# Kernel optimization log

Measured on AMD Instinct MI355X. Metric: run time of the kernel, lower is better.

## Reference

```python
import jax, jax.numpy as jnp
import numpy as np

NL, NQ, FD, HD, NH = 6, 128, 256, 512, 8
NC, B, T, H, W = 6, 1, 1, 48, 120
PPF = 24 // 6  # points_per_face
P = PPF * PPF * 6  # code emits (num_points//6)^2 points per face = 96 total
NPARAM, NTYPE, NATTR = 11, 10, 3
PMIN = np.array([-50., -50., -5., -15., -15., -5., -5., -3.14, 0.5, 0.5, 0.5], np.float32)
PMAX = np.array([50., 50., 5., 15., 15., 5., 5., 3.14, 10., 5., 3.], np.float32)


def _box_template():
    off = np.linspace(-0.4, 0.4, PPF).astype(np.float32)
    pts = []
    for axis in range(3):  # -x,+x,-y,+y,-z,+z faces, same order as torch code
        for s in (-0.5, 0.5):
            rem = [a for a in range(3) if a != axis]
            for i in range(PPF):
                for j in range(PPF):
                    p = [0.0, 0.0, 0.0]
                    p[axis] = s
                    p[rem[0]] = off[i]
                    p[rem[1]] = off[j]
                    pts.append(p)
    return np.asarray(pts, np.float32)  # [P,3]

TPL = _box_template()


def _mlp2(x, w1, b1, w2, b2):
    return jax.nn.relu(x @ w1.T + b1) @ w2.T + b2


def _ln(x, g, b):
    m = x.mean(-1, keepdims=True)
    v = ((x - m) ** 2).mean(-1, keepdims=True)
    return (x - m) * jax.lax.rsqrt(v + 1e-5) * g + b


def _mha(q, k, v, in_w, in_b, out_w, out_b):
    hd = HD // NH
    wq, wk, wv = jnp.split(in_w, 3, axis=0)
    bq, bk, bv = jnp.split(in_b, 3)
    def heads(x, w, b):
        y = x @ w.T + b
        return y.reshape(x.shape[0], x.shape[1], NH, hd).transpose(0, 2, 1, 3)
    Q, K, V = heads(q, wq, bq), heads(k, wk, bk), heads(v, wv, bv)
    a = jax.nn.softmax(jnp.einsum('bhqd,bhkd->bhqk', Q, K) * (hd ** -0.5), axis=-1)
    o = jnp.einsum('bhqk,bhkd->bhqd', a, V)
    o = o.transpose(0, 2, 1, 3).reshape(q.shape[0], q.shape[1], HD)
    return o @ out_w.T + out_b


def _sample_box_points(motion):
    # motion [B,N,11] -> [B,N,P,3]; indices: X0 Y1 Z2 .. YAW7 L8 W9 H10
    c = motion[..., 0:3]
    dims = motion[..., 8:11]
    yaw = motion[..., 7]
    p = TPL * dims[:, :, None, :]  # [B,N,P,3]
    cy, sy = jnp.cos(yaw)[..., None], jnp.sin(yaw)[..., None]
    xr = p[..., 0] * cy - p[..., 1] * sy
    yr = p[..., 0] * sy + p[..., 1] * cy
    return jnp.stack([xr, yr, p[..., 2]], -1) + c[:, :, None, :]


def _gather_aggregate(pts, features, proj):
    # pts [B,N,P,3]; features [NC,B,T,C,H,W]; proj [NC,3,4]
    Bb, N, Pp, _ = pts.shape
    NP = N * Pp
    hom = jnp.concatenate([pts, jnp.ones_like(pts[..., :1])], -1)
    feat_flat = features.reshape(NC, Bb, T, FD, H * W)
    acc = jnp.zeros((Bb, FD, NP), features.dtype)
    for cidx in range(NC):
        cam = jnp.einsum('ij,bnpj->bnpi', proj[cidx], hom)  # [B,N,P,3]
        z = cam[..., 2]
        zs = jnp.where(jnp.abs(z) > 1e-6, z, 1e-6)
        u = (cam[..., 0] / zs).reshape(Bb, NP)
        v = (cam[..., 1] / zs).reshape(Bb, NP)
        front = (z > 0).reshape(Bb, NP)
        u0, v0 = jnp.floor(u), jnp.floor(v)
        du, dv = u - u0, v - v0
        cam_acc = jnp.zeros((Bb, T, FD, NP), features.dtype)
        for (ui, vi, wgt) in ((u0, v0, (1 - du) * (1 - dv)),
                              (u0 + 1, v0, du * (1 - dv)),
                              (u0, v0 + 1, (1 - du) * dv),
                              (u0 + 1, v0 + 1, du * dv)):
            ok = front & (ui >= 0) & (ui <= W - 1) & (vi >= 0) & (vi <= H - 1)
            idx = (jnp.clip(vi, 0, H - 1) * W + jnp.clip(ui, 0, W - 1)).astype(jnp.int32)
            bidx = jnp.broadcast_to(idx[:, None, None, :], (Bb, T, FD, NP))
            g = jnp.take_along_axis(feat_flat[cidx], bidx, axis=-1)
            cam_acc = cam_acc + g * (wgt * ok)[:, None, None, :]
        acc = acc + cam_acc.mean(axis=1)  # mean over time
    agg = (acc / NC).reshape(Bb, FD, N, Pp).mean(-1)  # mean over cams and points
    return agg.transpose(0, 2, 1)  # [B,N,C]

_ga = jax.checkpoint(_gather_aggregate)


def _forward(features, proj, ego_states, queries0, param_min, param_max, motion_w1, motion_b1, motion_w2, motion_b2, type_w1, type_b1, type_w2, type_b2, attr_w1, attr_b1, attr_w2, attr_b2, fmlp_w1, fmlp_b1, fmlp_w2, fmlp_b2, sa_in_w, sa_in_b, sa_out_w, sa_out_b, fa_in_w, fa_in_b, fa_out_w, fa_out_b, ffn_w1, ffn_b1, ffn_w2, ffn_b2, ln1_g, ln1_b, ln2_g, ln2_b, ln3_g, ln3_b):
    Bb = features.shape[1]
    q = jnp.broadcast_to(queries0, (Bb, NQ, HD))
    preds = []
    for i in range(NL):
        motion = jax.nn.sigmoid(_mlp2(q, motion_w1, motion_b1, motion_w2, motion_b2)) * (param_max - param_min) + param_min
        tlog = _mlp2(q, type_w1, type_b1, type_w2, type_b2)
        attr = jax.nn.sigmoid(_mlp2(q, attr_w1, attr_b1, attr_w2, attr_b2))
        preds.append(jnp.concatenate([motion, tlog, attr], -1))
        if i == NL - 1:
            break  # last layer only predicts (layers[-1] unused, as in torch code)
        pts = _sample_box_points(motion)
        agg = _ga(pts, features, proj)
        feat_h = _mlp2(agg, fmlp_w1, fmlp_b1, fmlp_w2, fmlp_b2)
        x = _ln(q, ln1_g[i], ln1_b[i])
        x = x + _mha(x, x, x, sa_in_w[i], sa_in_b[i], sa_out_w[i], sa_out_b[i])
        x = _ln(x, ln2_g[i], ln2_b[i])
        x = x + _mha(x, feat_h, feat_h, fa_in_w[i], fa_in_b[i], fa_out_w[i], fa_out_b[i])
        x = _ln(x, ln3_g[i], ln3_b[i])
        q = x + _mlp2(x, ffn_w1[i], ffn_b1[i], ffn_w2[i], ffn_b2[i])
    return jnp.stack(preds)  # [NL,B,NQ,24]


def setup_inputs() -> dict:
    key = jax.random.key(0)
    ks = iter(jax.random.split(key, 64))
    def g(shape, s=0.02):
        return jax.random.normal(next(ks), shape, jnp.float32) * s
    fx, cx, cy = 40.0, W / 2.0, H / 2.0
    Ps = []
    for c in range(NC):
        th = 2.0 * np.pi * c / NC
        Rm = np.stack([np.array([-np.sin(th), np.cos(th), 0.0]),
                       np.array([0.0, 0.0, -1.0]),
                       np.array([np.cos(th), np.sin(th), 0.0])])
        K = np.array([[fx, 0.0, cx], [0.0, fx, cy], [0.0, 0.0, 1.0]])
        Pm = np.zeros((3, 4))
        Pm[:, :3] = K @ Rm
        Ps.append(Pm)
    inp = dict(
        features=jax.random.normal(next(ks), (NC, B, T, FD, H, W), jnp.float32),
        proj=jnp.asarray(np.asarray(Ps, np.float32)),
        ego_states=jax.random.normal(next(ks), (B, T, 5), jnp.float32),
        queries0=g((1, NQ, HD), 1.0),
        param_min=jnp.asarray(PMIN), param_max=jnp.asarray(PMAX),
        motion_w1=g((HD, HD)), motion_b1=jnp.zeros((HD,)),
        motion_w2=g((NPARAM, HD)), motion_b2=jnp.zeros((NPARAM,)),
        type_w1=g((HD, HD)), type_b1=jnp.zeros((HD,)),
        type_w2=g((NTYPE, HD)), type_b2=jnp.zeros((NTYPE,)),
        attr_w1=g((HD, HD)), attr_b1=jnp.zeros((HD,)),
        attr_w2=g((NATTR, HD)), attr_b2=jnp.zeros((NATTR,)),
        fmlp_w1=g((HD, FD)), fmlp_b1=jnp.zeros((HD,)),
        fmlp_w2=g((HD, HD)), fmlp_b2=jnp.zeros((HD,)),
        sa_in_w=g((NL, 3 * HD, HD)), sa_in_b=jnp.zeros((NL, 3 * HD)),
        sa_out_w=g((NL, HD, HD)), sa_out_b=jnp.zeros((NL, HD)),
        fa_in_w=g((NL, 3 * HD, HD)), fa_in_b=jnp.zeros((NL, 3 * HD)),
        fa_out_w=g((NL, HD, HD)), fa_out_b=jnp.zeros((NL, HD)),
        ffn_w1=g((NL, 4 * HD, HD)), ffn_b1=jnp.zeros((NL, 4 * HD)),
        ffn_w2=g((NL, HD, 4 * HD)), ffn_b2=jnp.zeros((NL, HD)),
        ln1_g=jnp.ones((NL, HD)), ln1_b=jnp.zeros((NL, HD)),
        ln2_g=jnp.ones((NL, HD)), ln2_b=jnp.zeros((NL, HD)),
        ln3_g=jnp.ones((NL, HD)), ln3_b=jnp.zeros((NL, HD)),
    )
    return inp


def reference(features, proj, ego_states, queries0, param_min, param_max, motion_w1, motion_b1, motion_w2, motion_b2, type_w1, type_b1, type_w2, type_b2, attr_w1, attr_b1, attr_w2, attr_b2, fmlp_w1, fmlp_b1, fmlp_w2, fmlp_b2, sa_in_w, sa_in_b, sa_out_w, sa_out_b, fa_in_w, fa_in_b, fa_out_w, fa_out_b, ffn_w1, ffn_b1, ffn_w2, ffn_b2, ln1_g, ln1_b, ln2_g, ln2_b, ln3_g, ln3_b):
    return _forward(features, proj, ego_states, queries0, param_min, param_max, motion_w1, motion_b1, motion_w2, motion_b2, type_w1, type_b1, type_w2, type_b2, attr_w1, attr_b1, attr_w2, attr_b2, fmlp_w1, fmlp_b1, fmlp_w2, fmlp_b2, sa_in_w, sa_in_b, sa_out_w, sa_out_b, fa_in_w, fa_in_b, fa_out_w, fa_out_b, ffn_w1, ffn_b1, ffn_w2, ffn_b2, ln1_g, ln1_b, ln2_g, ln2_b, ln3_g, ln3_b)
```

## Files before the change

kernel.cpp:

```cpp
#include <hip/hip_runtime.h>
#include <hip/hip_bf16.h>

typedef __hip_bfloat16 bf16;
typedef _Float16 h16;
typedef __attribute__((ext_vector_type(8))) _Float16 half8;
typedef __attribute__((ext_vector_type(4))) _Float16 half4;
typedef __attribute__((ext_vector_type(4))) float f32x4;

#define NQ 128
#define HD 512
#define FD 256
#define NC 6
#define IMH 48
#define IMW 120
#define HW 5760

__device__ __forceinline__ half8 pack8(float4 x, float4 y) {
    half8 h;
    h[0] = (h16)x.x; h[1] = (h16)x.y; h[2] = (h16)x.z; h[3] = (h16)x.w;
    h[4] = (h16)y.x; h[5] = (h16)y.y; h[6] = (h16)y.z; h[7] = (h16)y.w;
    return h;
}


__device__ __forceinline__ void transpose_body(int bx, int by, int cam,
                                               int tx, int ty, float* tile,
                                               const float* __restrict__ f,
                                               bf16* __restrict__ ft)
{
    int hw0 = bx * 32, fd0 = by * 32;
    const float* fb = f + (size_t)cam * FD * HW;
    for (int r = ty; r < 32; r += 8)
        tile[r * 33 + tx] = fb[(size_t)(fd0 + r) * HW + hw0 + tx];
    __syncthreads();
    bf16* fo = ft + (size_t)cam * HW * FD;
    for (int r = ty; r < 32; r += 8)
        fo[(size_t)(hw0 + r) * FD + fd0 + tx] = __float2bfloat16(tile[tx * 33 + r]);
}

struct SwzDesc {
    const float* src[11];
    unsigned int chunkStart[12];
    unsigned int tileStart[11];
    int K[11];
};

__device__ __forceinline__ int lperm(int lane, int ksl) {
    return lane ^ ((lane >> 4) & 3) ^ (ksl << 2);
}

__device__ __forceinline__ void swizzle_body(int bid, int t, h16* fbuf,
                                             const SwzDesc& d, h16* __restrict__ dst)
{
    int w = 0;
    while (bid >= (int)d.chunkStart[w + 1]) w++;
    int local = bid - (int)d.chunkStart[w];
    int Kk = d.K[w];
    int kc = Kk >> 6;
    int n64 = local / kc, kchunk = local - n64 * kc;

    int rr  = t >> 4;
    int cb  = (t & 15) * 4;
    int ksl = (t >> 3) & 1;
    int kk  = cb & 31;
    int laneb = ((kk >> 3) << 4) + rr;
    int elemB = (kk & 7) * 2;
    const float* sbase = d.src[w] + (size_t)(n64 * 64 + rr) * Kk + kchunk * 64 + cb;
#pragma unroll
    for (int rp = 0; rp < 4; rp++) {
        float4 u = *(const float4*)(sbase + (size_t)rp * 16 * Kk);
        int tile8 = ksl * 4 + rp;
        int l2 = lperm(laneb, ksl);
        half4* fp = (half4*)((char*)fbuf + tile8 * 1024 + l2 * 16 + elemB);
        half4 hv; hv[0] = (h16)u.x; hv[1] = (h16)u.y; hv[2] = (h16)u.z; hv[3] = (h16)u.w;
        *fp = hv;
    }
    __syncthreads();

    int K32 = Kk >> 5;
#pragma unroll
    for (int i = 0; i < 2; i++) {
        int hidx = t + i * 256;
        int tl = hidx >> 6, within = hidx & 63;
        int ksl2 = tl >> 2, ctt = tl & 3;
        int l2 = lperm(within, ksl2);
        size_t tileg = (size_t)d.tileStart[w]
                     + ((size_t)n64 * K32 + (kchunk * 2 + ksl2)) * 4 + ctt;
        *(half8*)(dst + tileg * 512 + within * 8) =
            *(const half8*)((const char*)fbuf + tl * 1024 + l2 * 16);
    }
}

template<int CTN, int NSUM, bool A2SW, bool LNA>
__device__ __forceinline__ void gemm_body(int bx, int by, int tid,
    float* redu, float* sst, float* sst2,
    const h16* __restrict__ A16, int lda, int sumStride,
    const float* __restrict__ A32,
    const float* __restrict__ lng, const float* __restrict__ lnb,
    float* __restrict__ lnout,
    const h16* __restrict__ A2_16, int a2Start,
    const h16* __restrict__ Wswz,
    const float* __restrict__ B0, const float* __restrict__ B1, const float* __restrict__ B2s,
    const float* __restrict__ R, int ldr,
    float* __restrict__ C32, h16* __restrict__ C16, int ldc,
    int K, int act)
{
    int w = tid >> 6, l = tid & 63;
    int lr = l & 15, q4 = l >> 4;
    int m0 = by * 16;
    int n0 = bx * 16 * CTN;
    int row = m0 + lr;
    int K32 = K >> 5;
    int KQ = K32 >> 2;
    int ks0 = w * KQ;

    bool useA2 = A2SW && (bx >= a2Start);

    const float* arow32 = nullptr;
    float mean = 0.f, rstd = 1.f;
    if (LNA && !useA2) {
        arow32 = A32 + (size_t)row * K + q4 * 8;
        float s = 0.f, s2 = 0.f;
        for (int ks = ks0; ks < ks0 + KQ; ks++) {
            float4 u = *(const float4*)(arow32 + ks * 32);
            float4 v = *(const float4*)(arow32 + ks * 32 + 4);
            s  += u.x + u.y + u.z + u.w + v.x + v.y + v.z + v.w;
            s2 += u.x*u.x + u.y*u.y + u.z*u.z + u.w*u.w
                + v.x*v.x + v.y*v.y + v.z*v.z + v.w*v.w;
        }
        s  += __shfl_xor(s, 16);  s  += __shfl_xor(s, 32);
        s2 += __shfl_xor(s2, 16); s2 += __shfl_xor(s2, 32);
        if (q4 == 0) { sst[w * 16 + lr] = s; sst2[w * 16 + lr] = s2; }
        __syncthreads();
        float st = sst[lr] + sst[16 + lr] + sst[32 + lr] + sst[48 + lr];
        float st2 = sst2[lr] + sst2[16 + lr] + sst2[32 + lr] + sst2[48 + lr];
        mean = st * (1.0f / (float)K);
        float var = st2 * (1.0f / (float)K) - mean * mean;
        rstd = rsqrtf(var + 1e-5f);
    }

    const h16* arow16 = nullptr;
    if (useA2)       arow16 = A2_16 + (size_t)row * 512 + q4 * 8;
    else if (!LNA)   arow16 = A16 + (size_t)row * lda + q4 * 8;

    const h16* wbase[CTN];
#pragma unroll
    for (int ct = 0; ct < CTN; ct++) {
        int tct = (n0 >> 4) + ct;
        wbase[ct] = Wswz + (((size_t)(tct >> 2) * K32 * 4 + (tct & 3)) * 64 + l) * 8;
    }

    f32x4 acc[CTN];
#pragma unroll
    for (int ct = 0; ct < CTN; ct++) acc[ct] = (f32x4){0.f, 0.f, 0.f, 0.f};

    bool wrln = LNA && !useA2 && (bx == 0) && lnout;

#pragma unroll 4
    for (int ks = ks0; ks < ks0 + KQ; ks++) {
        half8 a;
        if (LNA && !useA2) {
            float4 u = *(const float4*)(arow32 + ks * 32);
            float4 v = *(const float4*)(arow32 + ks * 32 + 4);
            float4 g0 = *(const float4*)(lng + ks * 32 + q4 * 8);
            float4 g1 = *(const float4*)(lng + ks * 32 + q4 * 8 + 4);
            float4 b0 = *(const float4*)(lnb + ks * 32 + q4 * 8);
            float4 b1 = *(const float4*)(lnb + ks * 32 + q4 * 8 + 4);
            float4 o0, o1;
            o0.x = (u.x - mean) * rstd * g0.x + b0.x;
            o0.y = (u.y - mean) * rstd * g0.y + b0.y;
            o0.z = (u.z - mean) * rstd * g0.z + b0.z;
            o0.w = (u.w - mean) * rstd * g0.w + b0.w;
            o1.x = (v.x - mean) * rstd * g1.x + b1.x;
            o1.y = (v.y - mean) * rstd * g1.y + b1.y;
            o1.z = (v.z - mean) * rstd * g1.z + b1.z;
            o1.w = (v.w - mean) * rstd * g1.w + b1.w;
            if (wrln) {
                *(float4*)(lnout + (size_t)row * K + ks * 32 + q4 * 8)     = o0;
                *(float4*)(lnout + (size_t)row * K + ks * 32 + q4 * 8 + 4) = o1;
            }
            a = pack8(o0, o1);
        } else if (NSUM == 1) {
            a = *(const half8*)(arow16 + (size_t)ks * 32);
        } else {
            float s[8] = {0.f, 0.f, 0.f, 0.f, 0.f, 0.f, 0.f, 0.f};
#pragma unroll
            for (int j = 0; j < NSUM; j++) {
                half8 tt = *(const half8*)(arow16 + (size_t)j * sumStride + ks * 32);
#pragma unroll
                for (int e = 0; e < 8; e++) s[e] += (float)tt[e];
            }
#pragma unroll
            for (int e = 0; e < 8; e++) a[e] = (h16)s[e];
        }
#pragma unroll
        for (int ct = 0; ct < CTN; ct++) {
            half8 bfr = *(const half8*)(wbase[ct] + (size_t)ks * 2048);
            acc[ct] = __builtin_amdgcn_mfma_f32_16x16x32_f16(a, bfr, acc[ct], 0, 0, 0);
        }
    }

#pragma unroll
    for (int ct = 0; ct < CTN; ct++)
        *(f32x4*)&redu[(size_t)(w * CTN + ct) * 256 + l * 4] = acc[ct];
    __syncthreads();

    if (w < CTN) {
        int ct = w;
        f32x4 sum = *(const f32x4*)&redu[(size_t)ct * 256 + l * 4];
#pragma unroll
        for (int w2 = 1; w2 < 4; w2++) {
            f32x4 tt = *(const f32x4*)&redu[(size_t)(w2 * CTN + ct) * 256 + l * 4];
            sum[0] += tt[0]; sum[1] += tt[1]; sum[2] += tt[2]; sum[3] += tt[3];
        }
        int n = n0 + ct * 16 + lr;
        float bv;
        if (B1) { int sec = n >> 9, ni = n & 511;
                  bv = (sec == 0) ? B0[ni] : (sec == 1 ? B1[ni] : B2s[ni]); }
        else bv = B0[n];
#pragma unroll
        for (int r = 0; r < 4; r++) {
            int m = m0 + q4 * 4 + r;
            float v = sum[r] + bv;
            if (act) v = fmaxf(v, 0.f);
            if (R) v += R[(size_t)m * ldr + n];
            if (C32) C32[(size_t)m * ldc + n] = v;
            if (C16) C16[(size_t)m * ldc + n] = (h16)v;
        }
    }
}

__device__ __forceinline__ void heads2_body(int q, int n, int lane,
    const h16* __restrict__ hid16,
    const float* __restrict__ w2m, const float* __restrict__ b2m,
    const float* __restrict__ w2t, const float* __restrict__ b2t,
    const float* __restrict__ w2a, const float* __restrict__ b2a,
    const float* __restrict__ pmin, const float* __restrict__ pmax,
    float* __restrict__ out)
{
    const float* wr; float bv; int mode, sect;
    if (n < 11)      { sect = 0; wr = w2m + n * 512;        bv = b2m[n];      mode = 0; }
    else if (n < 21) { sect = 1; wr = w2t + (n - 11) * 512; bv = b2t[n - 11]; mode = 1; }
    else             { sect = 2; wr = w2a + (n - 21) * 512; bv = b2a[n - 21]; mode = 2; }
    half8 hv = *(const half8*)(hid16 + q * 1536 + sect * 512 + lane * 8);
    const float4* w4 = (const float4*)(wr + lane * 8);
    float4 c0 = w4[0], c1 = w4[1];
    float acc = (float)hv[0] * c0.x + (float)hv[1] * c0.y
              + (float)hv[2] * c0.z + (float)hv[3] * c0.w
              + (float)hv[4] * c1.x + (float)hv[5] * c1.y
              + (float)hv[6] * c1.z + (float)hv[7] * c1.w;
    for (int off = 32; off; off >>= 1) acc += __shfl_xor(acc, off);
    if (lane == 0) {
        float v = acc + bv;
        if (mode == 0)      v = (1.0f / (1.0f + __expf(-v))) * (pmax[n] - pmin[n]) + pmin[n];
        else if (mode == 2) v = 1.0f / (1.0f + __expf(-v));
        out[q * 24 + n] = v;
    }
}

__device__ __forceinline__ void attn_body(int bid, int tid,
                                          float* KVl, float* Ql, float* Pl,
                                          const float* __restrict__ qkv,
                                          h16* __restrict__ out16)
{
    int h = bid >> 2, chunk = bid & 3;

    for (int l = tid; l < 2048; l += 256) {
        int row = l >> 4, c4 = (l & 15) * 4;
        float4 v = *(const float4*)&qkv[row * 1536 + 512 + h * 64 + c4];
        *(float4*)&KVl[row * 68 + c4] = v;
    }
    for (int l = tid; l < 512; l += 256) {
        int row = l >> 4, c4 = (l & 15) * 4;
        float4 v = *(const float4*)&qkv[(chunk * 32 + row) * 1536 + h * 64 + c4];
        *(float4*)&Ql[row * 68 + c4] = v;
    }
    __syncthreads();

    int w = tid >> 6, j = tid & 63;
    for (int r8 = 0; r8 < 8; r8++) {
        int lr = w * 8 + r8;
        float s0 = 0.f, s1 = 0.f;
#pragma unroll
        for (int k4 = 0; k4 < 64; k4 += 4) {
            float4 qv  = *(const float4*)&Ql[lr * 68 + k4];
            float4 k0v = *(const float4*)&KVl[j * 68 + k4];
            float4 k1v = *(const float4*)&KVl[(j + 64) * 68 + k4];
            s0 += qv.x * k0v.x + qv.y * k0v.y + qv.z * k0v.z + qv.w * k0v.w;
            s1 += qv.x * k1v.x + qv.y * k1v.y + qv.z * k1v.z + qv.w * k1v.w;
        }
        s0 *= 0.125f; s1 *= 0.125f;
        float m = fmaxf(s0, s1);
        for (int off = 32; off; off >>= 1) m = fmaxf(m, __shfl_xor(m, off));
        float e0 = __expf(s0 - m), e1 = __expf(s1 - m);
        float sm = e0 + e1;
        for (int off = 32; off; off >>= 1) sm += __shfl_xor(sm, off);
        float inv = 1.0f / sm;
        Pl[lr * 128 + j]      = e0 * inv;
        Pl[lr * 128 + j + 64] = e1 * inv;
    }
    __syncthreads();

    for (int l = tid; l < 2048; l += 256) {
        int row = l >> 4, c4 = (l & 15) * 4;
        float4 v = *(const float4*)&qkv[row * 1536 + 1024 + h * 64 + c4];
        KVl[(c4 + 0) * 132 + row] = v.x;
        KVl[(c4 + 1) * 132 + row] = v.y;
        KVl[(c4 + 2) * 132 + row] = v.z;
        KVl[(c4 + 3) * 132 + row] = v.w;
    }
    __syncthreads();

    int d = tid & 63, w2 = tid >> 6;
    for (int r8 = 0; r8 < 8; r8++) {
        int lr = w2 * 8 + r8;
        float o = 0.f;
#pragma unroll
        for (int j4 = 0; j4 < 128; j4 += 4) {
            float4 pv = *(const float4*)&Pl[lr * 128 + j4];
            float4 vv = *(const float4*)&KVl[d * 132 + j4];
            o += pv.x * vv.x + pv.y * vv.y + pv.z * vv.z + pv.w * vv.w;
        }
        out16[(chunk * 32 + lr) * 512 + h * 64 + d] = (h16)o;
    }
}


__global__ __launch_bounds__(256) void prep_k(SwzDesc d, h16* __restrict__ swz,
                                              const float* __restrict__ feat,
                                              bf16* __restrict__ feat_t,
                                              const float* __restrict__ q0,
                                              h16* __restrict__ q016)
{
    __shared__ char shm[8448];
    int bid = blockIdx.x, t = threadIdx.x;
    if (bid < 6432) {
        swizzle_body(bid, t, (h16*)shm, d, swz);
    } else if (bid < 15072) {
        int tb = bid - 6432;
        transpose_body(tb % 180, (tb / 180) % 8, tb / 1440, t & 31, t >> 5,
                       (float*)shm, feat, feat_t);
    } else {
        int i = (bid - 15072) * 256 + t;
        q016[i] = (h16)q0[i];
    }
}

template<int CTN, int NSUM, bool A2SW, bool LNA>
__global__ __launch_bounds__(256) void gemm_sk4(
    const h16* __restrict__ A16, int lda, int sumStride,
    const float* __restrict__ A32,
    const float* __restrict__ lng, const float* __restrict__ lnb,
    float* __restrict__ lnout,
    const h16* __restrict__ A2_16, int a2Start,
    const h16* __restrict__ Wswz,
    const float* __restrict__ B0, const float* __restrict__ B1, const float* __restrict__ B2s,
    const float* __restrict__ R, int ldr,
    float* __restrict__ C32, h16* __restrict__ C16, int ldc,
    int K, int act)
{
    __shared__ float redu[CTN * 4 * 256];
    __shared__ float sst[64], sst2[64];
    gemm_body<CTN, NSUM, A2SW, LNA>(blockIdx.x, blockIdx.y, threadIdx.x,
        redu, sst, sst2, A16, lda, sumStride, A32, lng, lnb, lnout, A2_16, a2Start,
        Wswz, B0, B1, B2s, R, ldr, C32, C16, ldc, K, act);
}

__global__ __launch_bounds__(64) void heads2_k(const h16* __restrict__ hid16,
                                               const float* __restrict__ w2m, const float* __restrict__ b2m,
                                               const float* __restrict__ w2t, const float* __restrict__ b2t,
                                               const float* __restrict__ w2a, const float* __restrict__ b2a,
                                               const float* __restrict__ pmin, const float* __restrict__ pmax,
                                               float* __restrict__ out)
{
    heads2_body(blockIdx.x, blockIdx.y, threadIdx.x,
                hid16, w2m, b2m, w2t, b2t, w2a, b2a, pmin, pmax, out);
}

__global__ __launch_bounds__(256) void attn_k(const float* __restrict__ qkv,
                                              h16* __restrict__ out16)
{
    __shared__ float KVl[128 * 68];
    __shared__ float Ql[32 * 68];
    __shared__ float Pl[32 * 128];
    attn_body(blockIdx.x, threadIdx.x, KVl, Ql, Pl, qkv, out16);
}

__global__ __launch_bounds__(256) void d2_k(
    const float* __restrict__ q32, const float* __restrict__ lng,
    const float* __restrict__ lnb, float* __restrict__ lnx,
    const h16* __restrict__ Wsain, const float* __restrict__ Bsain,
    float* __restrict__ qkv,
    const h16* __restrict__ hid16,
    const float* __restrict__ w2m, const float* __restrict__ b2m,
    const float* __restrict__ w2t, const float* __restrict__ b2t,
    const float* __restrict__ w2a, const float* __restrict__ b2a,
    const float* __restrict__ pmin, const float* __restrict__ pmax,
    float* __restrict__ out)
{
    __shared__ float redu[2 * 4 * 256];
    __shared__ float sst[64], sst2[64];
    int x = blockIdx.x, by = blockIdx.y, tid = threadIdx.x;
    if (x < 48) {
        gemm_body<2, 1, false, true>(x, by, tid, redu, sst, sst2,
            nullptr, 0, 0, q32, lng, lnb, lnx, nullptr, 0,
            Wsain, Bsain, nullptr, nullptr, nullptr, 0,
            qkv, nullptr, 1536, 512, 0);
    } else {
        int p = (((x - 48) * 8 + by) << 2) + (tid >> 6);
        heads2_body(p / 24, p % 24, tid & 63,
                    hid16, w2m, b2m, w2t, b2t, w2a, b2a, pmin, pmax, out);
    }
}

__global__ __launch_bounds__(256) void d4_k(
    const h16* __restrict__ agg16, const h16* __restrict__ Wf1,
    const float* __restrict__ Bf1, h16* __restrict__ fmlph16,
    const float* __restrict__ qkv, h16* __restrict__ attnb16)
{
    __shared__ float smem[14976];
    int x = blockIdx.x, by = blockIdx.y, tid = threadIdx.x;
    if (x < 32) {
        gemm_body<1, 6, false, false>(x, by, tid, smem, smem + 1024, smem + 1088,
            agg16, 256, 32768, nullptr, nullptr, nullptr, nullptr, nullptr, 0,
            Wf1, Bf1, nullptr, nullptr, nullptr, 0,
            nullptr, fmlph16, 512, 256, 1);
    } else {
        int slot = (x - 32) * 8 + by;
        attn_body(slot, tid, smem, smem + 8704, smem + 10880, qkv, attnb16);
    }
}

__global__ __launch_bounds__(256) void d5_k(
    const h16* __restrict__ fmlph16, const h16* __restrict__ Wf2,
    const float* __restrict__ Bf2, h16* __restrict__ feath16,
    const h16* __restrict__ attnb16, const h16* __restrict__ Wso,
    const float* __restrict__ Bso, const float* __restrict__ lnx,
    float* __restrict__ x1)
{
    __shared__ float redu[1024];
    __shared__ float sst[64], sst2[64];
    int x = blockIdx.x, by = blockIdx.y, tid = threadIdx.x;
    if (x < 32) {
        gemm_body<1, 1, false, false>(x, by, tid, redu, sst, sst2,
            fmlph16, 512, 0, nullptr, nullptr, nullptr, nullptr, nullptr, 0,
            Wf2, Bf2, nullptr, nullptr, nullptr, 0,
            nullptr, feath16, 512, 512, 0);
    } else {
        gemm_body<1, 1, false, false>(x - 32, by, tid, redu, sst, sst2,
            attnb16, 512, 0, nullptr, nullptr, nullptr, nullptr, nullptr, 0,
            Wso, Bso, nullptr, nullptr, lnx, 512,
            x1, nullptr, 512, 512, 0);
    }
}

__device__ __forceinline__ float bflo(unsigned u) {
    union { unsigned i; float f; } c; c.i = u << 16; return c.f;
}
__device__ __forceinline__ float bfhi(unsigned u) {
    union { unsigned i; float f; } c; c.i = u & 0xffff0000u; return c.f;
}

__global__ __launch_bounds__(256) void gather_k(const bf16* __restrict__ ft,
                                                const float* __restrict__ proj,
                                                const float* __restrict__ preds,
                                                h16* __restrict__ agg16)
{
    __shared__ float mo[11];
    __shared__ int   goff[384];
    __shared__ float gw[384];
    __shared__ int   cnt;
    __shared__ float part[8][256];
    int n = blockIdx.x, cam = blockIdx.y, tid = threadIdx.x;
    if (tid == 0) cnt = 0;
    if (tid < 11) mo[tid] = preds[n * 24 + tid];
    __syncthreads();

    if (tid < 96) {
        int p = tid;
        float dd0 = mo[8], dd1 = mo[9], dd2 = mo[10];
        float c0 = mo[0], c1 = mo[1], c2 = mo[2];
        float sy, cy;
        sincosf(mo[7], &sy, &cy);
        int face = p >> 4, axis = face >> 1;
        float sgn = (face & 1) ? 0.5f : -0.5f;
        float offi = -0.4f + (float)((p >> 2) & 3) * (0.8f / 3.0f);
        float offj = -0.4f + (float)(p & 3) * (0.8f / 3.0f);
        float t0, t1, t2;
        if (axis == 0)      { t0 = sgn;  t1 = offi; t2 = offj; }
        else if (axis == 1) { t0 = offi; t1 = sgn;  t2 = offj; }
        else                { t0 = offi; t1 = offj; t2 = sgn;  }
        float px = t0 * dd0, py = t1 * dd1, pz = t2 * dd2;
        float X = px * cy - py * sy + c0;
        float Y = px * sy + py * cy + c1;
        float Z = pz + c2;
        const float* P = proj + cam * 12;
        float cu = P[0] * X + P[1] * Y + P[2] * Z + P[3];
        float cv = P[4] * X + P[5] * Y + P[6] * Z + P[7];
        float cz = P[8] * X + P[9] * Y + P[10] * Z + P[11];
        float zs = (fabsf(cz) > 1e-6f) ? cz : 1e-6f;
        float u = cu / zs, v = cv / zs;
        bool front = cz > 0.0f;
        float u0 = floorf(u), v0 = floorf(v);
        float du = u - u0, dv = v - v0;
        float us[4] = {u0, u0 + 1.0f, u0, u0 + 1.0f};
        float vs[4] = {v0, v0, v0 + 1.0f, v0 + 1.0f};
        float wt[4] = {(1.0f - du) * (1.0f - dv), du * (1.0f - dv),
                       (1.0f - du) * dv, du * dv};
        int   myoff[4]; float myw[4]; int k = 0;
#pragma unroll
        for (int t = 0; t < 4; t++) {
            bool ok = front && (us[t] >= 0.0f) && (us[t] <= 119.0f)
                            && (vs[t] >= 0.0f) && (vs[t] <= 47.0f)
                            && (wt[t] > 0.0f);
            if (ok) {
                myoff[k] = ((int)vs[t] * IMW + (int)us[t]) * FD;
                myw[k]   = wt[t];
                k++;
            }
        }
        if (k) {
            int base = atomicAdd(&cnt, k);
            for (int s = 0; s < k; s++) { goff[base + s] = myoff[s]; gw[base + s] = myw[s]; }
        }
    }
    __syncthreads();
    int C = cnt;
    h16* slab = agg16 + (size_t)cam * 32768 + n * 256;
    if (C == 0) { slab[tid] = (h16)0.f; return; }

    int g8  = (tid & 31) * 8;
    int row = tid >> 5;
    const bf16* fb = ft + (size_t)cam * HW * FD + g8;
    float acc[8] = {0.f, 0.f, 0.f, 0.f, 0.f, 0.f, 0.f, 0.f};
    for (int e = row; e < C; e += 8) {
        float w = gw[e];
        uint4 rv = *(const uint4*)(fb + goff[e]);
        acc[0] += w * bflo(rv.x); acc[1] += w * bfhi(rv.x);
        acc[2] += w * bflo(rv.y); acc[3] += w * bfhi(rv.y);
        acc[4] += w * bflo(rv.z); acc[5] += w * bfhi(rv.z);
        acc[6] += w * bflo(rv.w); acc[7] += w * bfhi(rv.w);
    }
#pragma unroll
    for (int j = 0; j < 8; j++) part[row][g8 + j] = acc[j];
    __syncthreads();
    float s = 0.f;
#pragma unroll
    for (int r = 0; r < 8; r++) s += part[r][tid];
    slab[tid] = (h16)(s * (1.0f / 576.0f));
}

extern "C" void kernel_launch(void* const* d_in, const int* in_sizes, int n_in,
                              void* d_out, int out_size, void* d_ws, size_t ws_size,
                              hipStream_t stream)
{
    const float* features  = (const float*)d_in[0];
    const float* proj      = (const float*)d_in[1];
    const float* queries0  = (const float*)d_in[3];
    const float* pmin      = (const float*)d_in[4];
    const float* pmax      = (const float*)d_in[5];
    const float* motion_w1 = (const float*)d_in[6];
    const float* motion_b1 = (const float*)d_in[7];
    const float* motion_w2 = (const float*)d_in[8];
    const float* motion_b2 = (const float*)d_in[9];
    const float* type_w1   = (const float*)d_in[10];
    const float* type_b1   = (const float*)d_in[11];
    const float* type_w2   = (const float*)d_in[12];
    const float* type_b2   = (const float*)d_in[13];
    const float* attr_w1   = (const float*)d_in[14];
    const float* attr_b1   = (const float*)d_in[15];
    const float* attr_w2   = (const float*)d_in[16];
    const float* attr_b2   = (const float*)d_in[17];
    const float* fmlp_w1   = (const float*)d_in[18];
    const float* fmlp_b1   = (const float*)d_in[19];
    const float* fmlp_w2   = (const float*)d_in[20];
    const float* fmlp_b2   = (const float*)d_in[21];
    const float* sa_in_w   = (const float*)d_in[22];
    const float* sa_in_b   = (const float*)d_in[23];
    const float* sa_out_w  = (const float*)d_in[24];
    const float* sa_out_b  = (const float*)d_in[25];
    const float* fa_in_w   = (const float*)d_in[26];
    const float* fa_in_b   = (const float*)d_in[27];
    const float* fa_out_w  = (const float*)d_in[28];
    const float* fa_out_b  = (const float*)d_in[29];
    const float* ffn_w1    = (const float*)d_in[30];
    const float* ffn_b1    = (const float*)d_in[31];
    const float* ffn_w2    = (const float*)d_in[32];
    const float* ffn_b2    = (const float*)d_in[33];
    const float* ln1_g     = (const float*)d_in[34];
    const float* ln1_b     = (const float*)d_in[35];
    const float* ln2_g     = (const float*)d_in[36];
    const float* ln2_b     = (const float*)d_in[37];
    const float* ln3_g     = (const float*)d_in[38];
    const float* ln3_b     = (const float*)d_in[39];
    float* out = (float*)d_out;

    char* p = (char*)d_ws;
    bf16* feat_t = (bf16*)p;   p += (size_t)NC * HW * FD * 2;
    h16* swz     = (h16*)p;    p += (size_t)51456 * 512 * 2;
    h16* q016    = (h16*)p;    p += 65536 * 2;
    h16* hid16   = (h16*)p;    p += 196608 * 2;
    h16* agg16   = (h16*)p;    p += 196608 * 2;
    h16* fmlph16 = (h16*)p;    p += 65536 * 2;
    h16* feath16 = (h16*)p;    p += 65536 * 2;
    h16* attnb16 = (h16*)p;    p += 65536 * 2;
    h16* ffnh16  = (h16*)p;    p += 262144 * 2;
    h16* qn16    = (h16*)p;    p += 65536 * 2;
    float* qkv   = (float*)p;  p += 196608 * 4;
    float* lnx   = (float*)p;  p += 65536 * 4;
    float* x1    = (float*)p;  p += 65536 * 4;
    float* x2    = (float*)p;  p += 65536 * 4;
    float* qn32  = (float*)p;  p += 65536 * 4;

    SwzDesc sd;
    const float* srcs[11] = {motion_w1, type_w1, attr_w1, fmlp_w1, fmlp_w2,
                             sa_in_w, sa_out_w, fa_in_w, fa_out_w, ffn_w1, ffn_w2};
    int Ks[11]    = {512, 512, 512, 256, 512, 512, 512, 512, 512, 512, 2048};
    int tiles[11] = {512, 512, 512, 256, 512, 9216, 3072, 9216, 3072, 12288, 12288};
    unsigned int cumT = 0, cumC = 0;
    for (int i = 0; i < 11; i++) {
        sd.src[i] = srcs[i]; sd.K[i] = Ks[i];
        sd.tileStart[i] = cumT; sd.chunkStart[i] = cumC;
        cumT += tiles[i]; cumC += tiles[i] >> 3;
    }
    sd.chunkStart[11] = cumC;

    prep_k<<<15328, 256, 0, stream>>>(sd, swz, features, feat_t, queries0, q016);

    const h16* sw_heads = swz;
    const h16* sw_fmlp1 = swz + 786432;
    const h16* sw_fmlp2 = swz + 917504;
    const h16* sw_sain  = swz + 1179648;
    const h16* sw_saout = swz + 5898240;
    const h16* sw_fain  = swz + 7471104;
    const h16* sw_faout = swz + 12189696;
    const h16* sw_ffn1  = swz + 13762560;
    const h16* sw_ffn2  = swz + 20054016;

    const h16*   q16 = q016;
    const float* q32 = queries0;

    for (int i = 0; i < 6; i++) {
        gemm_sk4<2, 1, false, false><<<dim3(48, 8), 256, 0, stream>>>(
            q16, 512, 0, nullptr, nullptr, nullptr, nullptr, nullptr, 0,
            sw_heads, motion_b1, type_b1, attr_b1, nullptr, 0,
            nullptr, hid16, 1536, 512, 1);

        if (i == 5) {
            heads2_k<<<dim3(128, 24), 64, 0, stream>>>(hid16, motion_w2, motion_b2,
                                                       type_w2, type_b2, attr_w2, attr_b2,
                                                       pmin, pmax, out + i * 3072);
            break;
        }

        d2_k<<<dim3(144, 8), 256, 0, stream>>>(
            q32, ln1_g + i * 512, ln1_b + i * 512, lnx,
            sw_sain + (size_t)i * 786432, sa_in_b + i * 1536, qkv,
            hid16, motion_w2, motion_b2, type_w2, type_b2, attr_w2, attr_b2,
            pmin, pmax, out + i * 3072);

        gather_k<<<dim3(128, 6), 256, 0, stream>>>(feat_t, proj, out + i * 3072, agg16);

        d4_k<<<dim3(36, 8), 256, 0, stream>>>(
            agg16, sw_fmlp1, fmlp_b1, fmlph16, qkv, attnb16);

        d5_k<<<dim3(64, 8), 256, 0, stream>>>(
            fmlph16, sw_fmlp2, fmlp_b2, feath16,
            attnb16, sw_saout + (size_t)i * 262144, sa_out_b + i * 512, lnx, x1);

        gemm_sk4<2, 1, true, true><<<dim3(48, 8), 256, 0, stream>>>(
            nullptr, 0, 0, x1, ln2_g + i * 512, ln2_b + i * 512, lnx, feath16, 16,
            sw_fain + (size_t)i * 786432, fa_in_b + i * 1536, nullptr, nullptr,
            nullptr, 0, qkv, nullptr, 1536, 512, 0);

        attn_k<<<32, 256, 0, stream>>>(qkv, attnb16);

        gemm_sk4<1, 1, false, false><<<dim3(32, 8), 256, 0, stream>>>(
            attnb16, 512, 0, nullptr, nullptr, nullptr, nullptr, nullptr, 0,
            sw_faout + (size_t)i * 262144, fa_out_b + i * 512, nullptr, nullptr,
            lnx, 512, x2, nullptr, 512, 512, 0);

        gemm_sk4<2, 1, false, true><<<dim3(64, 8), 256, 0, stream>>>(
            nullptr, 0, 0, x2, ln3_g + i * 512, ln3_b + i * 512, lnx, nullptr, 0,
            sw_ffn1 + (size_t)i * 1048576, ffn_b1 + i * 2048, nullptr, nullptr,
            nullptr, 0, nullptr, ffnh16, 2048, 512, 1);

        gemm_sk4<1, 1, false, false><<<dim3(32, 8), 256, 0, stream>>>(
            ffnh16, 2048, 0, nullptr, nullptr, nullptr, nullptr, nullptr, 0,
            sw_ffn2 + (size_t)i * 1048576, ffn_b2 + i * 512, nullptr, nullptr,
            lnx, 512, qn32, qn16, 512, 2048, 0);

        q16 = qn16;
        q32 = qn32;
    }
}
```

Baseline: 815.1 us.

## Restructure prep kernel with grid-stride swizzle and 64x64 vectorized transpose

Replaces the one-block-per-chunk preprocessing kernel with a fixed 2160-block grid-stride kernel. The weight swizzle now goes straight from global memory to the fp16 tiled layout: each wave packs one tile with two float4 loads and one half8 store, with no shared-memory staging or barrier. The feature transpose moves from 32x32 to 64x64 shared tiles, with float4 loads and 16-byte packed bf16 stores. The aim is fewer, wider memory transactions and less launch and barrier overhead, at the cost of uncoalesced-stride source reads in the swizzle and more serial work per block.

```diff
diff --git a/kernel.cpp b/kernel.cpp
--- a/kernel.cpp
+++ b/kernel.cpp
@@ -22,72 +22,82 @@
     return h;
 }
 
-
-__device__ __forceinline__ void transpose_body(int bx, int by, int cam,
-                                               int tx, int ty, float* tile,
-                                               const float* __restrict__ f,
-                                               bf16* __restrict__ ft)
-{
-    int hw0 = bx * 32, fd0 = by * 32;
-    const float* fb = f + (size_t)cam * FD * HW;
-    for (int r = ty; r < 32; r += 8)
-        tile[r * 33 + tx] = fb[(size_t)(fd0 + r) * HW + hw0 + tx];
-    __syncthreads();
-    bf16* fo = ft + (size_t)cam * HW * FD;
-    for (int r = ty; r < 32; r += 8)
-        fo[(size_t)(hw0 + r) * FD + fd0 + tx] = __float2bfloat16(tile[tx * 33 + r]);
-}
-
 struct SwzDesc {
     const float* src[11];
-    unsigned int chunkStart[12];
-    unsigned int tileStart[11];
+    unsigned int tileStart[12];
     int K[11];
 };
 
-__device__ __forceinline__ int lperm(int lane, int ksl) {
-    return lane ^ ((lane >> 4) & 3) ^ (ksl << 2);
-}
-
-__device__ __forceinline__ void swizzle_body(int bid, int t, h16* fbuf,
-                                             const SwzDesc& d, h16* __restrict__ dst)
-{
-    int w = 0;
-    while (bid >= (int)d.chunkStart[w + 1]) w++;
-    int local = bid - (int)d.chunkStart[w];
-    int Kk = d.K[w];
-    int kc = Kk >> 6;
-    int n64 = local / kc, kchunk = local - n64 * kc;
-
-    int rr  = t >> 4;
-    int cb  = (t & 15) * 4;
-    int ksl = (t >> 3) & 1;
-    int kk  = cb & 31;
-    int laneb = ((kk >> 3) << 4) + rr;
-    int elemB = (kk & 7) * 2;
-    const float* sbase = d.src[w] + (size_t)(n64 * 64 + rr) * Kk + kchunk * 64 + cb;
-#pragma unroll
-    for (int rp = 0; rp < 4; rp++) {
-        float4 u = *(const float4*)(sbase + (size_t)rp * 16 * Kk);
-        int tile8 = ksl * 4 + rp;
-        int l2 = lperm(laneb, ksl);
-        half4* fp = (half4*)((char*)fbuf + tile8 * 1024 + l2 * 16 + elemB);
-        half4 hv; hv[0] = (h16)u.x; hv[1] = (h16)u.y; hv[2] = (h16)u.z; hv[3] = (h16)u.w;
-        *fp = hv;
-    }
-    __syncthreads();
-
-    int K32 = Kk >> 5;
-#pragma unroll
-    for (int i = 0; i < 2; i++) {
-        int hidx = t + i * 256;
-        int tl = hidx >> 6, within = hidx & 63;
-        int ksl2 = tl >> 2, ctt = tl & 3;
-        int l2 = lperm(within, ksl2);
-        size_t tileg = (size_t)d.tileStart[w]
-                     + ((size_t)n64 * K32 + (kchunk * 2 + ksl2)) * 4 + ctt;
-        *(half8*)(dst + tileg * 512 + within * 8) =
-            *(const half8*)((const char*)fbuf + tl * 1024 + l2 * 16);
+__global__ __launch_bounds__(256) void prep2_k(SwzDesc d, h16* __restrict__ swz,
+                                               const float* __restrict__ feat,
+                                               bf16* __restrict__ feat_t,
+                                               const float* __restrict__ q0,
+                                               h16* __restrict__ q016)
+{
+    __shared__ float tile[64 * 65];
+    int bid = blockIdx.x, t = threadIdx.x;
+
+    if (bid < 1536) {
+        int wid = bid * 4 + (t >> 6);
+        int l = t & 63;
+        int lr = l & 15, q8 = (l >> 4) * 8;
+        int total = (int)d.tileStart[11];
+#pragma unroll 2
+        for (int g = wid; g < total; g += 6144) {
+            int w = 0;
+            while (w < 10 && g >= (int)d.tileStart[w + 1]) w++;
+            int local = g - (int)d.tileStart[w];
+            int K = d.K[w];
+            int K32 = K >> 5;
+            int n64 = local / (K32 * 4);
+            int rem = local - n64 * (K32 * 4);
+            int ks = rem >> 2, ct = rem & 3;
+            int row = n64 * 64 + ct * 16 + lr;
+            int col = ks * 32 + q8;
+            const float* sp = d.src[w] + (size_t)row * K + col;
+            float4 u = *(const float4*)sp;
+            float4 v = *(const float4*)(sp + 4);
+            *(half8*)(swz + (size_t)g * 512 + l * 8) = pack8(u, v);
+        }
+    } else if (bid < 2152) {
+        for (int g = bid - 1536; g < 2160; g += 616) {
+            int cam = g / 360;
+            int r = g - cam * 360;
+            int fd_t = r / 90, hw_t = r - fd_t * 90;
+            int hw0 = hw_t * 64, fd0 = fd_t * 64;
+            const float* fb = feat + (size_t)cam * FD * HW;
+            int fr_b = t >> 4, c4 = (t & 15) * 4;
+#pragma unroll
+            for (int p = 0; p < 4; p++) {
+                int fr = p * 16 + fr_b;
+                float4 u = *(const float4*)&fb[(size_t)(fd0 + fr) * HW + hw0 + c4];
+                tile[fr * 65 + c4 + 0] = u.x;
+                tile[fr * 65 + c4 + 1] = u.y;
+                tile[fr * 65 + c4 + 2] = u.z;
+                tile[fr * 65 + c4 + 3] = u.w;
+            }
+            __syncthreads();
+            bf16* fo = feat_t + (size_t)cam * HW * FD;
+            int hr_b = t >> 3, j = t & 7;
+#pragma unroll
+            for (int s = 0; s < 2; s++) {
+                int hr = s * 32 + hr_b;
+                union { ushort us[8]; uint4 u4; } pk;
+#pragma unroll
+                for (int e = 0; e < 8; e++) {
+                    bf16 b = __float2bfloat16(tile[(j * 8 + e) * 65 + hr]);
+                    pk.us[e] = *(const ushort*)&b;
+                }
+                *(uint4*)&fo[(size_t)(hw0 + hr) * FD + fd0 + j * 8] = pk.u4;
+            }
+            __syncthreads();
+        }
+    } else {
+        for (int i = (bid - 2152) * 256 + t; i < 16384; i += 2048) {
+            float4 u = *(const float4*)(q0 + (size_t)i * 4);
+            half4 h; h[0] = (h16)u.x; h[1] = (h16)u.y; h[2] = (h16)u.z; h[3] = (h16)u.w;
+            *(half4*)(q016 + (size_t)i * 4) = h;
+        }
     }
 }
 
@@ -325,26 +335,6 @@
     }
 }
 
-
-__global__ __launch_bounds__(256) void prep_k(SwzDesc d, h16* __restrict__ swz,
-                                              const float* __restrict__ feat,
-                                              bf16* __restrict__ feat_t,
-                                              const float* __restrict__ q0,
-                                              h16* __restrict__ q016)
-{
-    __shared__ char shm[8448];
-    int bid = blockIdx.x, t = threadIdx.x;
-    if (bid < 6432) {
-        swizzle_body(bid, t, (h16*)shm, d, swz);
-    } else if (bid < 15072) {
-        int tb = bid - 6432;
-        transpose_body(tb % 180, (tb / 180) % 8, tb / 1440, t & 31, t >> 5,
-                       (float*)shm, feat, feat_t);
-    } else {
-        int i = (bid - 15072) * 256 + t;
-        q016[i] = (h16)q0[i];
-    }
-}
 
 template<int CTN, int NSUM, bool A2SW, bool LNA>
 __global__ __launch_bounds__(256) void gemm_sk4(
@@ -617,15 +607,15 @@
                              sa_in_w, sa_out_w, fa_in_w, fa_out_w, ffn_w1, ffn_w2};
     int Ks[11]    = {512, 512, 512, 256, 512, 512, 512, 512, 512, 512, 2048};
     int tiles[11] = {512, 512, 512, 256, 512, 9216, 3072, 9216, 3072, 12288, 12288};
-    unsigned int cumT = 0, cumC = 0;
+    unsigned int cumT = 0;
     for (int i = 0; i < 11; i++) {
         sd.src[i] = srcs[i]; sd.K[i] = Ks[i];
-        sd.tileStart[i] = cumT; sd.chunkStart[i] = cumC;
-        cumT += tiles[i]; cumC += tiles[i] >> 3;
-    }
-    sd.chunkStart[11] = cumC;
-
-    prep_k<<<15328, 256, 0, stream>>>(sd, swz, features, feat_t, queries0, q016);
+        sd.tileStart[i] = cumT;
+        cumT += tiles[i];
+    }
+    sd.tileStart[11] = cumT;
+
+    prep2_k<<<2160, 256, 0, stream>>>(sd, swz, features, feat_t, queries0, q016);
 
     const h16* sw_heads = swz;
     const h16* sw_fmlp1 = swz + 786432;
```

New measurement: 809.6 us. No clear change (-0.7%).
